# Performance work log

Measured on AMD Instinct MI355X. Metric: run time of the kernel, lower is better.

The kernel has to match this reference:

```python
import jax, jax.numpy as jnp
import numpy as np

B, H = 65536, 1024


def setup_inputs() -> dict:
    key = jax.random.key(0)
    ks = jax.random.split(key, 8)
    pos = jax.random.normal(ks[0], (B, 3), dtype=jnp.float32)
    quat = jax.random.normal(ks[1], (B, 4), dtype=jnp.float32)
    quat = quat / jnp.linalg.norm(quat, axis=-1, keepdims=True)
    gripper = jax.random.randint(ks[2], (B, 1), 0, 2).astype(jnp.float32)
    actions = jnp.concatenate([pos, quat, gripper], axis=-1)  # (B, 8)
    return {
        "actions": actions,
        "pos_W": jax.random.normal(ks[3], (3, H), dtype=jnp.float32) * 0.02,
        "pos_b": jnp.zeros((H,), dtype=jnp.float32),
        "rot_W": jax.random.normal(ks[4], (6, H), dtype=jnp.float32) * 0.02,
        "rot_b": jnp.zeros((H,), dtype=jnp.float32),
        "open_emb": jax.random.normal(ks[5], (2, H), dtype=jnp.float32) * 0.02,
        "ln_g": jnp.ones((H,), dtype=jnp.float32),
        "ln_b": jnp.zeros((H,), dtype=jnp.float32),
    }


def quat_to_euler_xyz(quat):
    # scipy R.from_quat uses (x, y, z, w); as_euler('xyz') = extrinsic x-y-z
    # (classic roll/pitch/yaw). Normalize like scipy does.
    quat = quat / jnp.linalg.norm(quat, axis=-1, keepdims=True)
    x, y, z, w = quat[..., 0], quat[..., 1], quat[..., 2], quat[..., 3]
    roll = jnp.arctan2(2.0 * (w * x + y * z), 1.0 - 2.0 * (x * x + y * y))
    pitch = jnp.arcsin(jnp.clip(2.0 * (w * y - z * x), -1.0, 1.0))
    yaw = jnp.arctan2(2.0 * (w * z + x * y), 1.0 - 2.0 * (y * y + z * z))
    return jnp.stack([roll, pitch, yaw], axis=-1)


def reference(actions, pos_W, pos_b, rot_W, rot_b, open_emb, ln_g, ln_b):
    pos_embeds = actions[..., :3] @ pos_W + pos_b
    open_idx = actions[..., 7].astype(jnp.int32)
    open_embeds = open_emb[open_idx]
    # original detaches quats (.data.cpu()) before conversion
    eul = quat_to_euler_xyz(jax.lax.stop_gradient(actions[..., 3:7]))
    rot_inputs = jnp.concatenate([jnp.sin(eul), jnp.cos(eul)], axis=-1)  # (B, 6)
    rot_embeds = rot_inputs @ rot_W + rot_b
    h = pos_embeds + rot_embeds + open_embeds
    mu = jnp.mean(h, axis=-1, keepdims=True)
    var = jnp.mean(jnp.square(h - mu), axis=-1, keepdims=True)
    return (h - mu) / jnp.sqrt(var + 1e-12) * ln_g + ln_b
```

## Files before the change

### kernel.cpp

```cpp
#include <hip/hip_runtime.h>
#include <math.h>


#define HDIM  1024
#define TPB   256
#define CPT   4
#define RPB   32
#define NB    11

typedef float v4f __attribute__((ext_vector_type(4)));

__device__ __forceinline__ float basis_val(
    int k, int c,
    const float* __restrict__ pos_W, const float* __restrict__ pos_b,
    const float* __restrict__ rot_W, const float* __restrict__ rot_b,
    const float* __restrict__ open_emb)
{
    if (k < 3)  return pos_W[k * HDIM + c];
    if (k < 9)  return rot_W[(k - 3) * HDIM + c];
    if (k == 9) return open_emb[HDIM + c] - open_emb[c];
    return pos_b[c] + rot_b[c] + open_emb[c];
}

__global__ __launch_bounds__(TPB) void gram_kernel(
    const float* __restrict__ pos_W, const float* __restrict__ pos_b,
    const float* __restrict__ rot_W, const float* __restrict__ rot_b,
    const float* __restrict__ open_emb, float* __restrict__ ws)
{
    __shared__ float s_part[4];
    const int b   = blockIdx.x;
    const int tid = threadIdx.x;
    float acc = 0.0f;
    if (b < NB * NB) {
        const int k = b / NB, l = b % NB;
        #pragma unroll
        for (int i = 0; i < HDIM / TPB; ++i) {
            const int c = tid + i * TPB;
            acc = fmaf(basis_val(k, c, pos_W, pos_b, rot_W, rot_b, open_emb),
                       basis_val(l, c, pos_W, pos_b, rot_W, rot_b, open_emb),
                       acc);
        }
    } else {
        const int k = b - NB * NB;
        #pragma unroll
        for (int i = 0; i < HDIM / TPB; ++i) {
            const int c = tid + i * TPB;
            acc += basis_val(k, c, pos_W, pos_b, rot_W, rot_b, open_emb);
        }
    }
    #pragma unroll
    for (int off = 32; off > 0; off >>= 1)
        acc += __shfl_xor(acc, off, 64);
    if ((tid & 63) == 0) s_part[tid >> 6] = acc;
    __syncthreads();
    if (tid == 0)
        ws[b] = (s_part[0] + s_part[1]) + (s_part[2] + s_part[3]);
}

__global__ __launch_bounds__(TPB, 4) void action_embed_kernel(
    const float* __restrict__ actions,
    const float* __restrict__ pos_W, const float* __restrict__ pos_b,
    const float* __restrict__ rot_W, const float* __restrict__ rot_b,
    const float* __restrict__ open_emb,
    const float* __restrict__ ln_g, const float* __restrict__ ln_b,
    const float* __restrict__ ws,
    float* __restrict__ out, int B)
{
    __shared__ float s_coef[RPB][12];

    const int tid  = threadIdx.x;
    const int col  = tid * CPT;
    const int row0 = blockIdx.x * RPB;

    const float4 wp0 = *(const float4*)(pos_W + 0 * HDIM + col);
    const float4 wp1 = *(const float4*)(pos_W + 1 * HDIM + col);
    const float4 wp2 = *(const float4*)(pos_W + 2 * HDIM + col);
    const float4 wr0 = *(const float4*)(rot_W + 0 * HDIM + col);
    const float4 wr1 = *(const float4*)(rot_W + 1 * HDIM + col);
    const float4 wr2 = *(const float4*)(rot_W + 2 * HDIM + col);
    const float4 wr3 = *(const float4*)(rot_W + 3 * HDIM + col);
    const float4 wr4 = *(const float4*)(rot_W + 4 * HDIM + col);
    const float4 wr5 = *(const float4*)(rot_W + 5 * HDIM + col);
    float4 bb, dopen;
    {
        const float4 pb = *(const float4*)(pos_b + col);
        const float4 rb = *(const float4*)(rot_b + col);
        const float4 o0 = *(const float4*)(open_emb + 0 * HDIM + col);
        const float4 o1 = *(const float4*)(open_emb + 1 * HDIM + col);
        bb    = make_float4(pb.x + rb.x + o0.x, pb.y + rb.y + o0.y,
                            pb.z + rb.z + o0.z, pb.w + rb.w + o0.w);
        dopen = make_float4(o1.x - o0.x, o1.y - o0.y, o1.z - o0.z, o1.w - o0.w);
    }
    const float4 g  = *(const float4*)(ln_g + col);
    const float4 bt = *(const float4*)(ln_b + col);

    if (tid < RPB) {
        const int r = row0 + tid;
        if (r < B) {
            const float4 a0 = *(const float4*)(actions + (size_t)r * 8);
            const float4 a1 = *(const float4*)(actions + (size_t)r * 8 + 4);
            float qx = a0.w, qy = a1.x, qz = a1.y, qw = a1.z;
            const float n = 1.0f / sqrtf(qx * qx + qy * qy + qz * qz + qw * qw);
            qx *= n; qy *= n; qz *= n; qw *= n;
            const float sr_n = 2.0f * (qw * qx + qy * qz);
            const float cr_n = 1.0f - 2.0f * (qx * qx + qy * qy);
            float sr, cr;
            {
                const float r2 = sr_n * sr_n + cr_n * cr_n;
                if (r2 < 1e-37f) { sr = 0.0f; cr = 1.0f; }
                else { const float ri = 1.0f / sqrtf(r2); sr = sr_n * ri; cr = cr_n * ri; }
            }
            float sp = 2.0f * (qw * qy - qz * qx);
            sp = fminf(1.0f, fmaxf(-1.0f, sp));
            const float cp = sqrtf(fmaxf(0.0f, 1.0f - sp * sp));
            const float sy_n = 2.0f * (qw * qz + qx * qy);
            const float cy_n = 1.0f - 2.0f * (qy * qy + qz * qz);
            float sy, cy;
            {
                const float r2 = sy_n * sy_n + cy_n * cy_n;
                if (r2 < 1e-37f) { sy = 0.0f; cy = 1.0f; }
                else { const float ri = 1.0f / sqrtf(r2); sy = sy_n * ri; cy = cy_n * ri; }
            }
            int idx = (int)a1.w;
            idx = idx < 0 ? 0 : (idx > 1 ? 1 : idx);

            float c[NB];
            c[0] = a0.x; c[1] = a0.y; c[2] = a0.z;
            c[3] = sr;   c[4] = sp;   c[5] = sy;
            c[6] = cr;   c[7] = cp;   c[8] = cy;
            c[9] = (float)idx;
            c[10] = 1.0f;

            float mdot = 0.0f;
            #pragma unroll
            for (int k = 0; k < NB; ++k)
                mdot = fmaf(c[k], ws[NB * NB + k], mdot);
            const float mu = mdot * (1.0f / HDIM);
            float q = 0.0f;
            #pragma unroll
            for (int k = 0; k < NB; ++k) {
                float t = 0.0f;
                #pragma unroll
                for (int l = 0; l < NB; ++l)
                    t = fmaf(ws[k * NB + l], c[l], t);
                q = fmaf(c[k], t, q);
            }
            float var = fmaf(q, 1.0f / HDIM, -mu * mu);
            var = fmaxf(var, 0.0f);
            const float rstd = 1.0f / sqrtf(var + 1e-12f);

            #pragma unroll
            for (int k = 0; k < 10; ++k)
                s_coef[tid][k] = c[k] * rstd;
            s_coef[tid][10] = rstd;
            s_coef[tid][11] = mu * rstd;
        }
    }
    __syncthreads();

    const int nrows = (B - row0 < RPB) ? (B - row0) : RPB;

    for (int rr = 0; rr < nrows; ++rr) {
        const float4 k0 = *(const float4*)&s_coef[rr][0];
        const float4 k1 = *(const float4*)&s_coef[rr][4];
        const float4 k2 = *(const float4*)&s_coef[rr][8];

        v4f o;
#define COMPONENT(f)                                                        \
        {                                                                   \
            float hh = fmaf(k2.z, bb.f, -k2.w);                             \
            hh = fmaf(k0.x, wp0.f, hh);                                     \
            hh = fmaf(k0.y, wp1.f, hh);                                     \
            hh = fmaf(k0.z, wp2.f, hh);                                     \
            hh = fmaf(k0.w, wr0.f, hh);                                     \
            hh = fmaf(k1.x, wr1.f, hh);                                     \
            hh = fmaf(k1.y, wr2.f, hh);                                     \
            hh = fmaf(k1.z, wr3.f, hh);                                     \
            hh = fmaf(k1.w, wr4.f, hh);                                     \
            hh = fmaf(k2.x, wr5.f, hh);                                     \
            hh = fmaf(k2.y, dopen.f, hh);                                   \
            o.f = fmaf(hh, g.f, bt.f);                                      \
        }
        COMPONENT(x) COMPONENT(y) COMPONENT(z) COMPONENT(w)
#undef COMPONENT
        __builtin_nontemporal_store(o,
            (v4f*)(out + (size_t)(row0 + rr) * HDIM + col));
    }
}

extern "C" void kernel_launch(void* const* d_in, const int* in_sizes, int n_in,
                              void* d_out, int out_size, void* d_ws, size_t ws_size,
                              hipStream_t stream) {
    const float* actions  = (const float*)d_in[0];
    const float* pos_W    = (const float*)d_in[1];
    const float* pos_b    = (const float*)d_in[2];
    const float* rot_W    = (const float*)d_in[3];
    const float* rot_b    = (const float*)d_in[4];
    const float* open_emb = (const float*)d_in[5];
    const float* ln_g     = (const float*)d_in[6];
    const float* ln_b     = (const float*)d_in[7];
    float* out = (float*)d_out;
    float* ws  = (float*)d_ws;

    const int B = in_sizes[0] / 8;
    hipLaunchKernelGGL(gram_kernel, dim3(NB * NB + NB), dim3(TPB), 0, stream,
                       pos_W, pos_b, rot_W, rot_b, open_emb, ws);
    const int grid = (B + RPB - 1) / RPB;
    hipLaunchKernelGGL(action_embed_kernel, dim3(grid), dim3(TPB), 0, stream,
                       actions, pos_W, pos_b, rot_W, rot_b, open_emb,
                       ln_g, ln_b, ws, out, B);
}
```

Before: 286.7 us.

## Double rows per block, unroll row loop by two, use plain stores

Doubles the rows handled per block from 32 to 64, halving the grid and spreading the per-block weight loads and quaternion setup over more rows. It drops the occupancy hint from launch_bounds. The output loop now handles two rows per iteration on full blocks, with a separate tail path. Nontemporal stores become ordinary stores, which may change cache behaviour on the write-bound 256MB output.

Result: faster. 276.0 us (-3.7%).

```diff
diff --git a/kernel.cpp b/kernel.cpp
--- a/kernel.cpp
+++ b/kernel.cpp
@@ -5,7 +5,7 @@
 #define HDIM  1024
 #define TPB   256
 #define CPT   4
-#define RPB   32
+#define RPB   64
 #define NB    11
 
 typedef float v4f __attribute__((ext_vector_type(4)));
@@ -57,7 +57,7 @@
         ws[b] = (s_part[0] + s_part[1]) + (s_part[2] + s_part[3]);
 }
 
-__global__ __launch_bounds__(TPB, 4) void action_embed_kernel(
+__global__ __launch_bounds__(TPB) void action_embed_kernel(
     const float* __restrict__ actions,
     const float* __restrict__ pos_W, const float* __restrict__ pos_b,
     const float* __restrict__ rot_W, const float* __restrict__ rot_b,
@@ -158,34 +158,56 @@
     }
     __syncthreads();
 
-    const int nrows = (B - row0 < RPB) ? (B - row0) : RPB;
-
-    for (int rr = 0; rr < nrows; ++rr) {
-        const float4 k0 = *(const float4*)&s_coef[rr][0];
-        const float4 k1 = *(const float4*)&s_coef[rr][4];
-        const float4 k2 = *(const float4*)&s_coef[rr][8];
-
-        v4f o;
-#define COMPONENT(f)                                                        \
+#define ROWCOMP(O, K0, K1, K2, f)                                           \
         {                                                                   \
-            float hh = fmaf(k2.z, bb.f, -k2.w);                             \
-            hh = fmaf(k0.x, wp0.f, hh);                                     \
-            hh = fmaf(k0.y, wp1.f, hh);                                     \
-            hh = fmaf(k0.z, wp2.f, hh);                                     \
-            hh = fmaf(k0.w, wr0.f, hh);                                     \
-            hh = fmaf(k1.x, wr1.f, hh);                                     \
-            hh = fmaf(k1.y, wr2.f, hh);                                     \
-            hh = fmaf(k1.z, wr3.f, hh);                                     \
-            hh = fmaf(k1.w, wr4.f, hh);                                     \
-            hh = fmaf(k2.x, wr5.f, hh);                                     \
-            hh = fmaf(k2.y, dopen.f, hh);                                   \
-            o.f = fmaf(hh, g.f, bt.f);                                      \
-        }
-        COMPONENT(x) COMPONENT(y) COMPONENT(z) COMPONENT(w)
-#undef COMPONENT
-        __builtin_nontemporal_store(o,
-            (v4f*)(out + (size_t)(row0 + rr) * HDIM + col));
-    }
+            float hh = fmaf(K2.z, bb.f, -K2.w);                             \
+            hh = fmaf(K0.x, wp0.f, hh);                                     \
+            hh = fmaf(K0.y, wp1.f, hh);                                     \
+            hh = fmaf(K0.z, wp2.f, hh);                                     \
+            hh = fmaf(K0.w, wr0.f, hh);                                     \
+            hh = fmaf(K1.x, wr1.f, hh);                                     \
+            hh = fmaf(K1.y, wr2.f, hh);                                     \
+            hh = fmaf(K1.z, wr3.f, hh);                                     \
+            hh = fmaf(K1.w, wr4.f, hh);                                     \
+            hh = fmaf(K2.x, wr5.f, hh);                                     \
+            hh = fmaf(K2.y, dopen.f, hh);                                   \
+            O.f = fmaf(hh, g.f, bt.f);                                      \
+        }
+#define ROW_ALL(O, K0, K1, K2)                                              \
+        ROWCOMP(O, K0, K1, K2, x) ROWCOMP(O, K0, K1, K2, y)                 \
+        ROWCOMP(O, K0, K1, K2, z) ROWCOMP(O, K0, K1, K2, w)
+
+    float* orow = out + (size_t)row0 * HDIM + col;
+
+    if (row0 + RPB <= B) {
+        for (int rr = 0; rr < RPB; rr += 2) {
+            const float4 a0 = *(const float4*)&s_coef[rr][0];
+            const float4 a1 = *(const float4*)&s_coef[rr][4];
+            const float4 a2 = *(const float4*)&s_coef[rr][8];
+            const float4 b0 = *(const float4*)&s_coef[rr + 1][0];
+            const float4 b1 = *(const float4*)&s_coef[rr + 1][4];
+            const float4 b2 = *(const float4*)&s_coef[rr + 1][8];
+            v4f oa, ob;
+            ROW_ALL(oa, a0, a1, a2);
+            ROW_ALL(ob, b0, b1, b2);
+            *(v4f*)orow = oa;
+            *(v4f*)(orow + HDIM) = ob;
+            orow += 2 * HDIM;
+        }
+    } else {
+        const int nrows = B - row0;
+        for (int rr = 0; rr < nrows; ++rr) {
+            const float4 a0 = *(const float4*)&s_coef[rr][0];
+            const float4 a1 = *(const float4*)&s_coef[rr][4];
+            const float4 a2 = *(const float4*)&s_coef[rr][8];
+            v4f oa;
+            ROW_ALL(oa, a0, a1, a2);
+            *(v4f*)orow = oa;
+            orow += HDIM;
+        }
+    }
+#undef ROW_ALL
+#undef ROWCOMP
 }
 
 extern "C" void kernel_launch(void* const* d_in, const int* in_sizes, int n_in,
```
